# Kernel optimization log

Measured on AMD Instinct MI355X. Metric: run time of the kernel, lower is better.

## Reference

```python
import jax, jax.numpy as jnp
import numpy as np


def _hadamard(n: int) -> np.ndarray:
    # Sylvester construction; n must be a power of 2 (asserted in the torch source).
    H = np.array([[1.0]], dtype=np.float32)
    while H.shape[0] < n:
        H = np.block([[H, H], [H, -H]])
    return (H * (n ** -0.5)).astype(np.float32)


def _rotate_activation(x):
    # hadamard_transform(x, scale=D**-0.5) over the last dim; bf16 in/out like the CUDA kernel.
    D = x.shape[-1]
    H = jnp.asarray(_hadamard(D))
    return (x.astype(jnp.float32) @ H).astype(x.dtype)


def _cu_seqlen_kv_bounds(seq_lens, num_ctx_tokens):
    # Vectorized equivalent of compute_cu_seqlen_kv_bounds_nocache (repeat_interleave -> searchsorted).
    offsets = jnp.concatenate([jnp.zeros(1, jnp.int32), jnp.cumsum(seq_lens).astype(jnp.int32)])
    pos = jnp.arange(num_ctx_tokens, dtype=jnp.int32)
    batch_ids = jnp.searchsorted(offsets, pos, side='right').astype(jnp.int32) - 1
    ks = offsets[batch_ids]                 # start of this token's sequence in packed KV
    ke = ks + (pos - ks) + 1                # causal: local_position + 1 past the start
    return ks, ke


def setup_inputs() -> dict:
    key = jax.random.key(0)
    k1, k2, k3 = jax.random.split(key, 3)
    T, H, D = 2048, 16, 128
    q = jax.random.normal(k1, (T, H, D), dtype=jnp.bfloat16)
    k = jax.random.normal(k2, (T, D), dtype=jnp.bfloat16)
    weights = jax.random.uniform(k3, (T, H), dtype=jnp.float32) * (H ** -0.5)
    seq_lens = jnp.array([1024, 1024], dtype=jnp.int32)
    return {"q": q, "k": k, "weights": weights, "seq_lens": seq_lens, "index_topk": 256}


def reference(q, k, weights, seq_lens, index_topk):
    T = q.shape[0]
    # Hadamard-rotate q and k (lightning indexer activation rotation).
    qr = _rotate_activation(q).astype(jnp.float32)   # [T, H, D]
    kr = _rotate_activation(k).astype(jnp.float32)   # [T, D]
    # Index score: I[t, s] = sum_h w[t, h] * relu(q[t, h] . k[s])
    logits = jnp.einsum('thd,sd->ths', qr, kr)       # [T, H, T]
    scores = jnp.einsum('ths,th->ts', jax.nn.relu(logits), weights)  # [T, T]
    # Causal ragged-batch KV window per token.
    ks, ke = _cu_seqlen_kv_bounds(seq_lens, T)
    pos = jnp.arange(T, dtype=jnp.int32)
    valid = (pos[None, :] >= ks[:, None]) & (pos[None, :] < ke[:, None])
    NEG = jnp.float32(-1e30)
    masked = jnp.where(valid, scores, NEG)
    topk_vals, topk_idx = jax.lax.top_k(masked, index_topk)  # [T, topk]
    return topk_vals, topk_idx
```

## Files before the change

### kernel.cpp

```cpp
#include <hip/hip_runtime.h>
#include <hip/hip_bf16.h>
#include <stdint.h>

typedef __attribute__((ext_vector_type(8))) short short8;
typedef __attribute__((ext_vector_type(4))) float float4_t;
typedef __attribute__((ext_vector_type(16))) float float16_t;

#define DDIM 128
#define SORTN 256
#define LROW 136
#define SCAP 1088
#define NCHT 17

__device__ inline unsigned short f32_to_bf16_rne(float f) {
    uint32_t u = __float_as_uint(f);
    return (unsigned short)((u + 0x7FFFu + ((u >> 16) & 1u)) >> 16);
}
__device__ inline float bf16_to_f32(unsigned short h) {
    return __uint_as_float(((uint32_t)h) << 16);
}
__device__ inline int ks_of(const int* seq_lens, int n_seq, int t) {
    int off = 0, r = 0;
    for (int i = 0; i < n_seq; ++i) {
        int nx = off + seq_lens[i];
        if (t < nx) { r = off; break; }
        off = nx;
    }
    return r;
}

__device__ inline int wave_reduce_add_dpp(int x) {
    x += __builtin_amdgcn_update_dpp(0, x, 0x111, 0xF, 0xF, true);
    x += __builtin_amdgcn_update_dpp(0, x, 0x112, 0xF, 0xF, true);
    x += __builtin_amdgcn_update_dpp(0, x, 0x114, 0xF, 0xF, true);
    x += __builtin_amdgcn_update_dpp(0, x, 0x118, 0xF, 0xF, true);
    x += __builtin_amdgcn_update_dpp(0, x, 0x142, 0xA, 0xF, true);
    x += __builtin_amdgcn_update_dpp(0, x, 0x143, 0xC, 0xF, true);
    return __builtin_amdgcn_readlane(x, 63);
}

__global__ __launch_bounds__(256) void rotate_k_kernel(
        const unsigned short* __restrict__ k, unsigned short* __restrict__ kr, int T) {
    int row = blockIdx.x * 16 + (threadIdx.x >> 4);
    if (row >= T) return;
    int l16 = threadIdx.x & 15;
    short8 in = *(const short8*)(k + (size_t)row * DDIM + 8 * l16);
    float f[8];
    #pragma unroll
    for (int j = 0; j < 8; ++j) f[j] = bf16_to_f32((unsigned short)in[j]);
    #pragma unroll
    for (int b = 1; b <= 4; b <<= 1)
        #pragma unroll
        for (int j = 0; j < 8; ++j)
            if (!(j & b)) { float a = f[j], c = f[j | b]; f[j] = a + c; f[j | b] = a - c; }
    #pragma unroll
    for (int m = 1; m <= 8; m <<= 1) {
        bool hi = (l16 & m) != 0;
        #pragma unroll
        for (int j = 0; j < 8; ++j) {
            float o = __shfl_xor(f[j], m, 64);
            f[j] = hi ? (o - f[j]) : (f[j] + o);
        }
    }
    const float sc = 0.08838834764831845f;
    short8 out;
    #pragma unroll
    for (int j = 0; j < 8; ++j) out[j] = (short)f32_to_bf16_rne(f[j] * sc);
    *(short8*)(kr + (size_t)row * DDIM + 8 * l16) = out;
}

__global__ __launch_bounds__(256, 2) void fused_kernel(
        const unsigned short* __restrict__ q,
        const unsigned short* __restrict__ kr,
        const float* __restrict__ w,
        const int* __restrict__ seq_lens, int n_seq,
        float* __restrict__ out_vals, float* __restrict__ out_idx,
        int T, int H, int K, int Tt) {
    __shared__ __align__(16) unsigned short bL[128 * LROW];
    __shared__ __align__(16) float scw[4][SCAP];
    unsigned short* qst = (unsigned short*)&scw[0][0];

    const int tid  = threadIdx.x;
    const int wv   = tid >> 6, lane = tid & 63;
    const int col  = lane & 15, kgrp = lane >> 4;
    const int hi   = lane >> 5;
    const int l31  = lane & 31;
    const int srow = tid >> 4, sseg = tid & 15;

    const int m     = blockIdx.x;
    const int halfG = Tt >> 1;
    const int ttile = (Tt <= 1) ? 0 : ((m < halfG) ? m : (Tt - 1 - (m - halfG)));
    const int tt0   = ttile * 4;

    const int tg1 = tt0 + 1, tg2 = tt0 + 2, tg3 = tt0 + 3;
    const bool v0 = (tt0 < T), v1 = (tg1 < T), v2 = (tg2 < T), v3 = (tg3 < T);
    const int t0 = v0 ? tt0 : T - 1, t1 = v1 ? tg1 : T - 1;
    const int t2 = v2 ? tg2 : T - 1, t3 = v3 ? tg3 : T - 1;
    const int ks0 = ks_of(seq_lens, n_seq, t0);
    const int ks1 = ks_of(seq_lens, n_seq, t1);
    const int ks2 = ks_of(seq_lens, n_seq, t2);
    const int ks3 = ks_of(seq_lens, n_seq, t3);

    const int bks    = ks_of(seq_lens, n_seq, tt0);
    const int bke    = (tt0 + 4 < T) ? (tt0 + 4) : T;
    const int nchunk = (bke - bks + 127) >> 7;

    short8 pre[8];
    #pragma unroll
    for (int i = 0; i < 8; ++i) {
        int gs = bks + srow + 16 * i; if (gs > T - 1) gs = T - 1;
        pre[i] = *(const short8*)(kr + (size_t)gs * DDIM + sseg * 8);
    }

    const int t_r = (tt0 + wv < T) ? (tt0 + wv) : (T - 1);
    float f[4][8];
    const unsigned short* qrow = q + ((size_t)t_r * H + col) * DDIM + kgrp * 8;
    #pragma unroll
    for (int kk = 0; kk < 4; ++kk) {
        short8 v = *(const short8*)(qrow + kk * 32);
        #pragma unroll
        for (int j = 0; j < 8; ++j) f[kk][j] = bf16_to_f32((unsigned short)v[j]);
    }
    #pragma unroll
    for (int b = 1; b <= 4; b <<= 1)
        #pragma unroll
        for (int kk = 0; kk < 4; ++kk)
            #pragma unroll
            for (int j = 0; j < 8; ++j)
                if (!(j & b)) { float a = f[kk][j], c = f[kk][j | b];
                                f[kk][j] = a + c; f[kk][j | b] = a - c; }
    #pragma unroll
    for (int kk = 0; kk < 4; ++kk)
        #pragma unroll
        for (int j = 0; j < 8; ++j) {
            float o = __shfl_xor(f[kk][j], 16, 64);
            f[kk][j] = (kgrp & 1) ? (o - f[kk][j]) : (f[kk][j] + o);
        }
    #pragma unroll
    for (int kk = 0; kk < 4; ++kk)
        #pragma unroll
        for (int j = 0; j < 8; ++j) {
            float o = __shfl_xor(f[kk][j], 32, 64);
            f[kk][j] = (kgrp & 2) ? (o - f[kk][j]) : (f[kk][j] + o);
        }
    #pragma unroll
    for (int j = 0; j < 8; ++j) {
        { float a = f[0][j], c = f[1][j]; f[0][j] = a + c; f[1][j] = a - c; }
        { float a = f[2][j], c = f[3][j]; f[2][j] = a + c; f[3][j] = a - c; }
        { float a = f[0][j], c = f[2][j]; f[0][j] = a + c; f[2][j] = a - c; }
        { float a = f[1][j], c = f[3][j]; f[1][j] = a + c; f[3][j] = a - c; }
    }
    const float scl = 0.08838834764831845f;
    #pragma unroll
    for (int kk = 0; kk < 4; ++kk) {
        short8 o;
        #pragma unroll
        for (int j = 0; j < 8; ++j) o[j] = (short)f32_to_bf16_rne(f[kk][j] * scl);
        *(short8*)&qst[(wv * 16 + col) * LROW + kgrp * 8 + kk * 32] = o;
    }
    __syncthreads();

    short8 afrag0[8], afrag1[8];
    {
        const unsigned short* qr0 = qst + l31 * LROW + hi * 8;
        const unsigned short* qr1 = qst + (32 + l31) * LROW + hi * 8;
        #pragma unroll
        for (int k8 = 0; k8 < 8; ++k8) {
            afrag0[k8] = *(const short8*)(qr0 + 16 * k8);
            afrag1[k8] = *(const short8*)(qr1 + 16 * k8);
        }
    }
    float w0r[8], w1r[8], w2r[8], w3r[8];
    #pragma unroll
    for (int r = 0; r < 8; ++r) {
        int h = (r & 3) + 8 * ((r >> 2) & 1) + 4 * hi;
        w0r[r] = w[(size_t)t0 * H + h];
        w1r[r] = w[(size_t)t1 * H + h];
        w2r[r] = w[(size_t)t2 * H + h];
        w3r[r] = w[(size_t)t3 * H + h];
    }
    __syncthreads();

    const int nrow = wv * 32 + l31;
    for (int c = 0; c < nchunk; ++c) {
        const int kv0 = bks + (c << 7);
        #pragma unroll
        for (int i = 0; i < 8; ++i)
            *(short8*)&bL[(srow + 16 * i) * LROW + sseg * 8] = pre[i];
        __syncthreads();
        if (c + 1 < nchunk) {
            int kvn = kv0 + 128;
            #pragma unroll
            for (int i = 0; i < 8; ++i) {
                int gs = kvn + srow + 16 * i; if (gs > T - 1) gs = T - 1;
                pre[i] = *(const short8*)(kr + (size_t)gs * DDIM + sseg * 8);
            }
        }
        const unsigned short* brow = &bL[nrow * LROW + hi * 8];
        float16_t acc01 = {0.f, 0.f, 0.f, 0.f, 0.f, 0.f, 0.f, 0.f,
                           0.f, 0.f, 0.f, 0.f, 0.f, 0.f, 0.f, 0.f};
        float16_t acc23 = {0.f, 0.f, 0.f, 0.f, 0.f, 0.f, 0.f, 0.f,
                           0.f, 0.f, 0.f, 0.f, 0.f, 0.f, 0.f, 0.f};
        __builtin_amdgcn_s_setprio(1);
        #pragma unroll
        for (int k8 = 0; k8 < 8; ++k8) {
            short8 bf = *(const short8*)(brow + 16 * k8);
            acc01 = __builtin_amdgcn_mfma_f32_32x32x16_bf16(afrag0[k8], bf, acc01, 0, 0, 0);
            acc23 = __builtin_amdgcn_mfma_f32_32x32x16_bf16(afrag1[k8], bf, acc23, 0, 0, 0);
        }
        __builtin_amdgcn_s_setprio(0);
        float p0 = 0.f, p1 = 0.f, p2 = 0.f, p3 = 0.f;
        #pragma unroll
        for (int r = 0; r < 8; ++r) {
            float a = acc01[r];     a = a > 0.f ? a : 0.f; p0 += w0r[r] * a;
            float b = acc01[r + 8]; b = b > 0.f ? b : 0.f; p1 += w1r[r] * b;
            float g = acc23[r];     g = g > 0.f ? g : 0.f; p2 += w2r[r] * g;
            float d = acc23[r + 8]; d = d > 0.f ? d : 0.f; p3 += w3r[r] * d;
        }
        p0 += __shfl_xor(p0, 32, 64);
        p1 += __shfl_xor(p1, 32, 64);
        p2 += __shfl_xor(p2, 32, 64);
        p3 += __shfl_xor(p3, 32, 64);
        const int s = kv0 + nrow;
        if (hi == 0) {
            if (v0 && s >= ks0 && s <= t0) scw[0][s - ks0] = p0;
            if (v2 && s >= ks2 && s <= t2) scw[2][s - ks2] = p2;
        } else {
            if (v1 && s >= ks1 && s <= t1) scw[1][s - ks1] = p1;
            if (v3 && s >= ks3 && s <= t3) scw[3][s - ks3] = p3;
        }
        __syncthreads();
    }

    const int t_s = tt0 + wv;
    if (t_s >= T) return;
    const int ks_w = ks_of(seq_lens, n_seq, t_s);
    const int ke_w = t_s + 1;
    const int n    = ke_w - ks_w;

    const int nch = (n + 63) >> 6;
    uint32_t ukey[NCHT];
    #pragma unroll
    for (int c = 0; c < NCHT; ++c) {
        if (c < nch) {
            int i = c * 64 + lane;
            ukey[c] = (i < n) ? __float_as_uint(scw[wv][i]) : 0u;
        } else ukey[c] = 0u;
    }
    unsigned long long* candw = (unsigned long long*)&scw[wv][0];

    const int Keff = (n < K) ? n : K;
    uint32_t ustar = 0;
    int ttake = K;
    if (n > K) {
        uint32_t lo = 0, hia = 0x80000000u;
        for (int it = 0; it < 31; ++it) {
            uint32_t mid = (lo + hia) >> 1;
            int lc = 0;
            #pragma unroll
            for (int c = 0; c < NCHT; ++c)
                if (c < nch) lc += (ukey[c] >= mid) ? 1 : 0;
            int total = wave_reduce_add_dpp(lc);
            if (total >= K) lo = mid; else hia = mid;
        }
        ustar = lo;
        int lg = 0;
        #pragma unroll
        for (int c = 0; c < NCHT; ++c)
            if (c < nch) lg += (ukey[c] > ustar) ? 1 : 0;
        ttake = K - wave_reduce_add_dpp(lg);
    }

    {
        const unsigned long long ltm = (1ull << lane) - 1ull;
        int base = 0, tieBase = 0;
        const bool selAll = (n <= K);
        #pragma unroll
        for (int c = 0; c < NCHT; ++c) {
            if (c < nch) {
                int i = c * 64 + lane;
                bool inb = (i < n);
                uint32_t u = ukey[c];
                bool isGt  = inb && (selAll || u > ustar);
                bool isTie = inb && !selAll && (u == ustar);
                unsigned long long mt = __ballot(isTie);
                int tr = tieBase + (int)__popcll(mt & ltm);
                bool take = isGt || (isTie && tr < ttake);
                unsigned long long mk = __ballot(take);
                if (take) {
                    int pos = base + (int)__popcll(mk & ltm);
                    int s = ks_w + i;
                    if (pos < SORTN)
                        candw[pos] = ((((unsigned long long)u << 11) |
                                       (unsigned long long)(T - 1 - s)) + 1ull);
                }
                base    += (int)__popcll(mk);
                tieBase += (int)__popcll(mt);
            }
        }
        for (int i = Keff + lane; i < SORTN; i += 64) candw[i] = 0ull;
    }

    unsigned long long kreg[4];
    #pragma unroll
    for (int r = 0; r < 4; ++r) kreg[r] = candw[4 * lane + r];

    #define CX(a, b, dsc) { unsigned long long _mx = (a) > (b) ? (a) : (b); \
                            unsigned long long _mn = (a) > (b) ? (b) : (a); \
                            (a) = (dsc) ? _mx : _mn; (b) = (dsc) ? _mn : _mx; }
    #pragma unroll
    for (int size = 2; size <= SORTN; size <<= 1) {
        #pragma unroll
        for (int stride = SORTN >> 1; stride >= 4; stride >>= 1) {
            if (stride > (size >> 1)) continue;
            int lmask = stride >> 2;
            #pragma unroll
            for (int r = 0; r < 4; ++r) {
                int e = 4 * lane + r;
                unsigned long long other = __shfl_xor(kreg[r], lmask, 64);
                bool desc = ((e & size) == 0);
                bool iAmLow = ((e & stride) == 0);
                bool keepMax = (iAmLow == desc);
                kreg[r] = keepMax ? (kreg[r] > other ? kreg[r] : other)
                                  : (kreg[r] < other ? kreg[r] : other);
            }
        }
        if (size >= 4) {
            bool d = (((4 * lane) & size) == 0);
            CX(kreg[0], kreg[2], d);
            CX(kreg[1], kreg[3], d);
            CX(kreg[0], kreg[1], d);
            CX(kreg[2], kreg[3], d);
        } else {
            CX(kreg[0], kreg[1], true);
            CX(kreg[2], kreg[3], false);
        }
    }
    #undef CX

    if (4 * lane < K) {
        float4_t v4, i4;
        #pragma unroll
        for (int r = 0; r < 4; ++r) {
            int e = 4 * lane + r;
            unsigned long long key = kreg[r];
            float v; int idx;
            if (key != 0ull) {
                unsigned long long km1 = key - 1ull;
                v = __uint_as_float((uint32_t)(km1 >> 11));
                idx = T - 1 - (int)(km1 & 0x7FFull);
            } else {
                int pidx = e - Keff;
                idx = (pidx < ks_w) ? pidx : (ke_w + (pidx - ks_w));
                v = -1e30f;
            }
            v4[r] = v; i4[r] = (float)idx;
        }
        *(float4_t*)(out_vals + (size_t)t_s * K + 4 * lane) = v4;
        *(float4_t*)(out_idx  + (size_t)t_s * K + 4 * lane) = i4;
    }
}

extern "C" void kernel_launch(void* const* d_in, const int* in_sizes, int n_in,
                              void* d_out, int out_size, void* d_ws, size_t ws_size,
                              hipStream_t stream) {
    const unsigned short* q = (const unsigned short*)d_in[0];
    const unsigned short* k = (const unsigned short*)d_in[1];
    const float* w          = (const float*)d_in[2];
    const int* seq_lens     = (const int*)d_in[3];
    const int n_seq = in_sizes[3];
    const int T = in_sizes[1] / DDIM;
    const int H = in_sizes[2] / T;
    const int K = out_size / (2 * T);

    unsigned short* kr = (unsigned short*)d_ws;
    float* out_vals = (float*)d_out;
    float* out_idx  = out_vals + (size_t)T * K;

    rotate_k_kernel<<<dim3((T + 15) / 16), dim3(256), 0, stream>>>(k, kr, T);
    const int Tt = (T + 3) / 4;
    fused_kernel<<<dim3(Tt), dim3(256), 0, stream>>>(
        q, kr, w, seq_lens, n_seq, out_vals, out_idx, T, H, K, Tt);
}
```

Baseline: 99.73 us.

## Stage K tiles with global_load_lds into XOR-swizzled LDS and ballot-count top-k

Replaces the register-prefetched, padded-row LDS staging of rotated K with direct global-to-LDS 16-byte loads. These write into an unpadded 128-wide tile whose 16-byte segments are XOR-swizzled by row. The q staging buffer and the MFMA fragment reads use the same swizzle. This removes the VGPR round trip, the padding and some LDS footprint. The trade-off is that the next tile is now loaded after compute and waited on, rather than prefetched during it. The threshold binary search in top-k also replaces the DPP wave reduction with per-chunk ballot plus popcount, and the score buffer capacity is trimmed to 1024.

Measured after the change: 105.6 us. 5.9% more time.

```diff
diff --git a/kernel.cpp b/kernel.cpp
--- a/kernel.cpp
+++ b/kernel.cpp
@@ -8,9 +8,8 @@
 
 #define DDIM 128
 #define SORTN 256
-#define LROW 136
-#define SCAP 1088
-#define NCHT 17
+#define SCAP 1024
+#define NCHT 16
 
 __device__ inline unsigned short f32_to_bf16_rne(float f) {
     uint32_t u = __float_as_uint(f);
@@ -29,14 +28,10 @@
     return r;
 }
 
-__device__ inline int wave_reduce_add_dpp(int x) {
-    x += __builtin_amdgcn_update_dpp(0, x, 0x111, 0xF, 0xF, true);
-    x += __builtin_amdgcn_update_dpp(0, x, 0x112, 0xF, 0xF, true);
-    x += __builtin_amdgcn_update_dpp(0, x, 0x114, 0xF, 0xF, true);
-    x += __builtin_amdgcn_update_dpp(0, x, 0x118, 0xF, 0xF, true);
-    x += __builtin_amdgcn_update_dpp(0, x, 0x142, 0xA, 0xF, true);
-    x += __builtin_amdgcn_update_dpp(0, x, 0x143, 0xC, 0xF, true);
-    return __builtin_amdgcn_readlane(x, 63);
+__device__ inline void gll16(const unsigned short* src, unsigned short* ldsdst) {
+    __builtin_amdgcn_global_load_lds(
+        (const __attribute__((address_space(1))) void*)src,
+        (__attribute__((address_space(3))) void*)ldsdst, 16, 0, 0);
 }
 
 __global__ __launch_bounds__(256) void rotate_k_kernel(
@@ -76,7 +71,7 @@
         const int* __restrict__ seq_lens, int n_seq,
         float* __restrict__ out_vals, float* __restrict__ out_idx,
         int T, int H, int K, int Tt) {
-    __shared__ __align__(16) unsigned short bL[128 * LROW];
+    __shared__ __align__(16) unsigned short bL[128 * 128];
     __shared__ __align__(16) float scw[4][SCAP];
     unsigned short* qst = (unsigned short*)&scw[0][0];
 
@@ -85,7 +80,6 @@
     const int col  = lane & 15, kgrp = lane >> 4;
     const int hi   = lane >> 5;
     const int l31  = lane & 31;
-    const int srow = tid >> 4, sseg = tid & 15;
 
     const int m     = blockIdx.x;
     const int halfG = Tt >> 1;
@@ -105,12 +99,18 @@
     const int bke    = (tt0 + 4 < T) ? (tt0 + 4) : T;
     const int nchunk = (bke - bks + 127) >> 7;
 
-    short8 pre[8];
-    #pragma unroll
-    for (int i = 0; i < 8; ++i) {
-        int gs = bks + srow + 16 * i; if (gs > T - 1) gs = T - 1;
-        pre[i] = *(const short8*)(kr + (size_t)gs * DDIM + sseg * 8);
-    }
+    #define STAGE(kv0_) do {                                                  \
+        _Pragma("unroll")                                                     \
+        for (int i_ = 0; i_ < 8; ++i_) {                                      \
+            const int r_ = wv * 32 + 4 * i_ + (lane >> 4);                    \
+            int grow_ = (kv0_) + r_; if (grow_ > T - 1) grow_ = T - 1;        \
+            const int gcol_ = (lane & 15) ^ (r_ & 15);                        \
+            gll16(kr + (size_t)grow_ * DDIM + gcol_ * 8,                      \
+                  &bL[(wv * 32 + 4 * i_) * 128]);                             \
+        }                                                                     \
+    } while (0)
+
+    STAGE(bks);
 
     const int t_r = (tt0 + wv < T) ? (tt0 + wv) : (T - 1);
     float f[4][8];
@@ -156,18 +156,19 @@
         short8 o;
         #pragma unroll
         for (int j = 0; j < 8; ++j) o[j] = (short)f32_to_bf16_rne(f[kk][j] * scl);
-        *(short8*)&qst[(wv * 16 + col) * LROW + kgrp * 8 + kk * 32] = o;
+        const int sp = (kgrp + 4 * kk) ^ col;
+        *(short8*)&qst[(wv * 16 + col) * 128 + (sp << 3)] = o;
     }
     __syncthreads();
 
     short8 afrag0[8], afrag1[8];
     {
-        const unsigned short* qr0 = qst + l31 * LROW + hi * 8;
-        const unsigned short* qr1 = qst + (32 + l31) * LROW + hi * 8;
+        const int nr15 = l31 & 15;
         #pragma unroll
         for (int k8 = 0; k8 < 8; ++k8) {
-            afrag0[k8] = *(const short8*)(qr0 + 16 * k8);
-            afrag1[k8] = *(const short8*)(qr1 + 16 * k8);
+            const int sp = (hi + 2 * k8) ^ nr15;
+            afrag0[k8] = *(const short8*)&qst[l31 * 128 + (sp << 3)];
+            afrag1[k8] = *(const short8*)&qst[(32 + l31) * 128 + (sp << 3)];
         }
     }
     float w0r[8], w1r[8], w2r[8], w3r[8];
@@ -182,21 +183,9 @@
     __syncthreads();
 
     const int nrow = wv * 32 + l31;
+    const int nr15 = l31 & 15;
     for (int c = 0; c < nchunk; ++c) {
         const int kv0 = bks + (c << 7);
-        #pragma unroll
-        for (int i = 0; i < 8; ++i)
-            *(short8*)&bL[(srow + 16 * i) * LROW + sseg * 8] = pre[i];
-        __syncthreads();
-        if (c + 1 < nchunk) {
-            int kvn = kv0 + 128;
-            #pragma unroll
-            for (int i = 0; i < 8; ++i) {
-                int gs = kvn + srow + 16 * i; if (gs > T - 1) gs = T - 1;
-                pre[i] = *(const short8*)(kr + (size_t)gs * DDIM + sseg * 8);
-            }
-        }
-        const unsigned short* brow = &bL[nrow * LROW + hi * 8];
         float16_t acc01 = {0.f, 0.f, 0.f, 0.f, 0.f, 0.f, 0.f, 0.f,
                            0.f, 0.f, 0.f, 0.f, 0.f, 0.f, 0.f, 0.f};
         float16_t acc23 = {0.f, 0.f, 0.f, 0.f, 0.f, 0.f, 0.f, 0.f,
@@ -204,7 +193,8 @@
         __builtin_amdgcn_s_setprio(1);
         #pragma unroll
         for (int k8 = 0; k8 < 8; ++k8) {
-            short8 bf = *(const short8*)(brow + 16 * k8);
+            const int sp = (hi + 2 * k8) ^ nr15;
+            short8 bf = *(const short8*)&bL[nrow * 128 + (sp << 3)];
             acc01 = __builtin_amdgcn_mfma_f32_32x32x16_bf16(afrag0[k8], bf, acc01, 0, 0, 0);
             acc23 = __builtin_amdgcn_mfma_f32_32x32x16_bf16(afrag1[k8], bf, acc23, 0, 0, 0);
         }
@@ -230,7 +220,12 @@
             if (v3 && s >= ks3 && s <= t3) scw[3][s - ks3] = p3;
         }
         __syncthreads();
-    }
+        if (c + 1 < nchunk) {
+            STAGE(kv0 + 128);
+            __syncthreads();
+        }
+    }
+    #undef STAGE
 
     const int t_s = tt0 + wv;
     if (t_s >= T) return;
@@ -256,19 +251,18 @@
         uint32_t lo = 0, hia = 0x80000000u;
         for (int it = 0; it < 31; ++it) {
             uint32_t mid = (lo + hia) >> 1;
-            int lc = 0;
+            int total = 0;
             #pragma unroll
             for (int c = 0; c < NCHT; ++c)
-                if (c < nch) lc += (ukey[c] >= mid) ? 1 : 0;
-            int total = wave_reduce_add_dpp(lc);
+                if (c < nch) total += (int)__popcll(__ballot(ukey[c] >= mid));
             if (total >= K) lo = mid; else hia = mid;
         }
         ustar = lo;
-        int lg = 0;
+        int tg = 0;
         #pragma unroll
         for (int c = 0; c < NCHT; ++c)
-            if (c < nch) lg += (ukey[c] > ustar) ? 1 : 0;
-        ttake = K - wave_reduce_add_dpp(lg);
+            if (c < nch) tg += (int)__popcll(__ballot(ukey[c] > ustar));
+        ttake = K - tg;
     }
 
     {
```
